# Kernel optimization log

Hardware: AMD Instinct MI355X
Metric: run time of the kernel (lower is better)

The kernel has to match this reference:

```python
import jax, jax.numpy as jnp
import numpy as np

WINDOW_SIZE = 11
SIGMA = 1.5
C1 = 0.01 ** 2
C2 = 0.03 ** 2


def _gaussian_window(window_size, sigma, channel, dtype):
    x = np.arange(window_size)
    g = np.exp(-((x - window_size // 2) ** 2) / (2.0 * sigma ** 2))
    g = g / g.sum()
    w2d = np.outer(g, g).astype(np.float32)  # [K,K]
    # depthwise kernel: [C, 1, K, K] (OIHW with feature_group_count=C)
    w = np.broadcast_to(w2d, (channel, 1, window_size, window_size))
    return jnp.asarray(w, dtype=dtype)


def _blur(x, window, channel):
    pad = WINDOW_SIZE // 2
    return jax.lax.conv_general_dilated(
        x, window,
        window_strides=(1, 1),
        padding=[(pad, pad), (pad, pad)],
        dimension_numbers=('NCHW', 'OIHW', 'NCHW'),
        feature_group_count=channel,
    )


def setup_inputs() -> dict:
    key = jax.random.key(0)
    k1, k2 = jax.random.split(key)
    shape = (16, 3, 512, 512)
    img1 = jax.random.uniform(k1, shape, dtype=jnp.float32)
    img2 = jax.random.uniform(k2, shape, dtype=jnp.float32)
    return {"img1": img1, "img2": img2}


def reference(img1, img2):
    channel = img1.shape[1]
    window = _gaussian_window(WINDOW_SIZE, SIGMA, channel, img1.dtype)

    mu1 = _blur(img1, window, channel)
    mu2 = _blur(img2, window, channel)
    mu1_sq = mu1 * mu1
    mu2_sq = mu2 * mu2
    mu1_mu2 = mu1 * mu2

    sigma1_sq = _blur(img1 * img1, window, channel) - mu1_sq
    sigma2_sq = _blur(img2 * img2, window, channel) - mu2_sq
    sigma12 = _blur(img1 * img2, window, channel) - mu1_mu2

    ssim_map = ((2.0 * mu1_mu2 + C1) * (2.0 * sigma12 + C2)) / (
        (mu1_sq + mu2_sq + C1) * (sigma1_sq + sigma2_sq + C2))
    return jnp.mean(ssim_map)  # size_average=True
```

## Files before the change

kernel.cpp:

```cpp
#include <hip/hip_runtime.h>
#include <math.h>

typedef float v2 __attribute__((ext_vector_type(2)));

#define SCALE 1073741824.0
#define NPIX 12582912.0
#define C1f 1e-4f
#define C2f 9e-4f

struct Wts {
    float w[11];
    v2 hp[12];
};

__device__ __forceinline__ v2 sp(float x) { v2 r; r.x = x; r.y = x; return r; }
__device__ __forceinline__ v2 f2(v2 a, v2 b, v2 c) {
    return __builtin_elementwise_fma(a, b, c);
}

#define LOADP(Abuf, Bbuf, grow) do {                                        \
    int rc_ = (grow); rc_ = rc_ < 0 ? 0 : (rc_ > 511 ? 511 : rc_);          \
    const float* ra_ = baseA + rc_ * 512;                                   \
    const float* rb_ = baseB + rc_ * 512;                                   \
    _Pragma("unroll") for (int k_ = 0; k_ < 7; ++k_) {                      \
        Abuf[k_] = *(const v2*)(ra_ + off[k_]);                             \
        Bbuf[k_] = *(const v2*)(rb_ + off[k_]);                             \
    } } while (0)

#define HPM(Abuf, Bbuf, PH, mval) do {                                      \
    v2 hS_ = sp(0.f), hD_ = sp(0.f), hP_ = sp(0.f), hM_ = sp(0.f);          \
    _Pragma("unroll") for (int j_ = 0; j_ < 12; ++j_) {                     \
        const int e_ = j_ + 1;                                              \
        const float xa_ = (e_ & 1) ? Abuf[e_ >> 1].y : Abuf[e_ >> 1].x;     \
        const float xb_ = (e_ & 1) ? Bbuf[e_ >> 1].y : Bbuf[e_ >> 1].x;     \
        const float u_ = xa_ + xb_, v_ = xa_ - xb_;                         \
        hS_ = f2(hpl[j_], sp(u_), hS_);                                     \
        hD_ = f2(hpl[j_], sp(v_), hD_);                                     \
        hP_ = f2(hpl[j_], sp(u_ * u_), hP_);                                \
        hM_ = f2(hpl[j_], sp(v_ * v_), hM_);                                \
    }                                                                       \
    const v2 mm_ = sp(mval);                                                \
    rS[PH] = hS_ * mm_; rD[PH] = hD_ * mm_;                                 \
    rP[PH] = hP_ * mm_; rM[PH] = hM_ * mm_; } while (0)

#define VOUTM(PH, vmval) do {                                               \
    v2 S_ = sp(0.f), D_ = sp(0.f), P_ = sp(0.f), M_ = sp(0.f);              \
    _Pragma("unroll") for (int k_ = 0; k_ < 11; ++k_) {                     \
        const int q_ = ((PH) + 1 + k_) % 12;                                \
        const v2 wk_ = sp(W.w[k_]);                                         \
        S_ = f2(wk_, rS[q_], S_); D_ = f2(wk_, rD[q_], D_);                 \
        P_ = f2(wk_, rP[q_], P_); M_ = f2(wk_, rM[q_], M_);                 \
    }                                                                       \
    const v2 ss_ = S_ * S_, dd_ = D_ * D_;                                  \
    const v2 mu12_  = (ss_ - dd_) * sp(0.25f);                              \
    const v2 musq_  = (ss_ + dd_) * sp(0.5f);                               \
    const v2 sig12_ = (P_ - M_) * sp(0.25f) - mu12_;                        \
    const v2 sigsm_ = (P_ + M_) * sp(0.5f) - musq_;                         \
    const v2 num_ = (sp(2.f) * mu12_ + sp(C1f)) * (sp(2.f) * sig12_ + sp(C2f)); \
    const v2 den_ = (musq_ + sp(C1f)) * (sigsm_ + sp(C2f));                 \
    v2 r_;                                                                  \
    r_.x = __builtin_amdgcn_rcpf(den_.x);                                   \
    r_.y = __builtin_amdgcn_rcpf(den_.y);                                   \
    r_ = r_ * (sp(2.f) - den_ * r_);                                        \
    loc = f2(num_ * sp(vmval), r_, loc); } while (0)

#define PSTEP(PH, PAR) do {                                                 \
    const float m_ = (X >= 0 && X < 512) ? 1.f : 0.f;                       \
    if (PAR) { HPM(A1, B1, PH, m_); LOADP(A1, B1, X + 2); }                 \
    else     { HPM(A0, B0, PH, m_); LOADP(A0, B0, X + 2); }                 \
    ++X;                                                                    \
    __builtin_amdgcn_sched_barrier(0); } while (0)

#define MSTEP(PH, PAR) do {                                                 \
    const float vm_ = (X - 6 < 512) ? 1.f : 0.f;                            \
    VOUTM(PH, vm_);                                                         \
    const float m_ = (X < 512) ? 1.f : 0.f;                                 \
    if (PAR) { HPM(A1, B1, PH, m_); LOADP(A1, B1, X + 2); }                 \
    else     { HPM(A0, B0, PH, m_); LOADP(A0, B0, X + 2); }                 \
    ++X;                                                                    \
    __builtin_amdgcn_sched_barrier(0); } while (0)

__global__ __launch_bounds__(256, 2) void ssim_main(
    const float* __restrict__ img1, const float* __restrict__ img2,
    unsigned long long* __restrict__ acc, Wts W)
{
    __shared__ float red[4];
    const int tid = threadIdx.x;
    const int lane = tid & 63;
    const int wv = tid >> 6;
    const int r0 = blockIdx.x * 48;
    const int plane = blockIdx.y;
    const int c = wv * 128 + 2 * lane;

    const float* baseA = img1 + (size_t)plane * 262144;
    const float* baseB = img2 + (size_t)plane * 262144;

    int off[7];
#pragma unroll
    for (int k = 0; k < 7; ++k) {
        int o = c - 6 + 2 * k;
        off[k] = o < 0 ? 0 : (o > 510 ? 510 : o);
    }
    v2 hpl[12];
#pragma unroll
    for (int j = 0; j < 12; ++j) {
        const int col = c - 5 + j;
        hpl[j] = (col >= 0 && col < 512) ? W.hp[j] : sp(0.f);
    }

    v2 rS[12], rD[12], rP[12], rM[12];
    v2 A0[7], B0[7], A1[7], B1[7];
    v2 loc = sp(0.f);

    int X = r0 - 5;
    LOADP(A0, B0, r0 - 5);
    LOADP(A1, B1, r0 - 4);
    __builtin_amdgcn_sched_barrier(0);

    PSTEP(0, 0);  PSTEP(1, 1);  PSTEP(2, 0);  PSTEP(3, 1);
    PSTEP(4, 0);  PSTEP(5, 1);  PSTEP(6, 0);  PSTEP(7, 1);
    PSTEP(8, 0);  PSTEP(9, 1);  PSTEP(10, 0);

    for (int b = 0; b < 4; ++b) {
        MSTEP(11, 1); MSTEP(0, 0);  MSTEP(1, 1);  MSTEP(2, 0);
        MSTEP(3, 1);  MSTEP(4, 0);  MSTEP(5, 1);  MSTEP(6, 0);
        MSTEP(7, 1);  MSTEP(8, 0);  MSTEP(9, 1);  MSTEP(10, 0);
    }

    float l = loc.x + loc.y;
#pragma unroll
    for (int o2 = 32; o2; o2 >>= 1)
        l += __shfl_down(l, o2, 64);
    if (lane == 0) red[wv] = l;
    __syncthreads();
    if (tid == 0) {
        const float bs = red[0] + red[1] + red[2] + red[3];
        const unsigned long long q =
            (unsigned long long)__double2ll_rn((double)bs * SCALE);
        atomicAdd(acc, q);
    }
}

__global__ void ssim_final(const unsigned long long* __restrict__ acc,
                           float* __restrict__ out)
{
    if (threadIdx.x == 0)
        out[0] = (float)((double)(*acc) * (1.0 / SCALE) / NPIX);
}

extern "C" void kernel_launch(void* const* d_in, const int* in_sizes, int n_in,
                              void* d_out, int out_size, void* d_ws, size_t ws_size,
                              hipStream_t stream) {
    const float* img1 = (const float*)d_in[0];
    const float* img2 = (const float*)d_in[1];
    float* out = (float*)d_out;
    unsigned long long* acc = (unsigned long long*)d_ws;

    double g[11], ssum = 0.0;
    for (int i = 0; i < 11; ++i) {
        const double d = (double)(i - 5);
        g[i] = exp(-(d * d) / 4.5);
        ssum += g[i];
    }
    Wts W;
    for (int i = 0; i < 11; ++i) W.w[i] = (float)(g[i] / ssum);
    for (int j = 0; j < 12; ++j) {
        v2 p;
        p.x = (j <= 10) ? W.w[j] : 0.f;
        p.y = (j >= 1) ? W.w[j - 1] : 0.f;
        W.hp[j] = p;
    }

    hipMemsetAsync(d_ws, 0, sizeof(unsigned long long), stream);
    ssim_main<<<dim3(11, 48), 256, 0, stream>>>(img1, img2, acc, W);
    ssim_final<<<1, 64, 0, stream>>>(acc, out);
}
```

Measured before the change: 84.36 us.

## Stage image rows through double-buffered LDS and shrink row tiles

Each block now loads one row of both images per step with coalesced float4 global loads into a double-buffered LDS slot that carries zero-padded halos. Each thread then reads its 14-column window from LDS instead of issuing overlapping, clamped global loads, and the squared sum/difference terms are computed once per loaded element. Row tiles shrink from 48 to 36, which gives more blocks (15x48), and the launch bound rises to 3 blocks per CU. In exchange there is a __syncthreads every row step and more vertical halo recomputation per tile.

```diff
diff --git a/kernel.cpp b/kernel.cpp
--- a/kernel.cpp
+++ b/kernel.cpp
@@ -8,6 +8,9 @@
 #define C1f 1e-4f
 #define C2f 9e-4f
 
+#define IMG_STR  528
+#define SLOT_STR 1056
+
 struct Wts {
     float w[11];
     v2 hp[12];
@@ -18,30 +21,32 @@
     return __builtin_elementwise_fma(a, b, c);
 }
 
-#define LOADP(Abuf, Bbuf, grow) do {                                        \
-    int rc_ = (grow); rc_ = rc_ < 0 ? 0 : (rc_ > 511 ? 511 : rc_);          \
-    const float* ra_ = baseA + rc_ * 512;                                   \
-    const float* rb_ = baseB + rc_ * 512;                                   \
+#define HPM(PH, SLR) do {                                                   \
+    const float* rp_ = &rowbuf[(SLR) * SLOT_STR] + lds_rd;                  \
+    v2 ca_[7], cb_[7];                                                      \
     _Pragma("unroll") for (int k_ = 0; k_ < 7; ++k_) {                      \
-        Abuf[k_] = *(const v2*)(ra_ + off[k_]);                             \
-        Bbuf[k_] = *(const v2*)(rb_ + off[k_]);                             \
-    } } while (0)
-
-#define HPM(Abuf, Bbuf, PH, mval) do {                                      \
+        ca_[k_] = *(const v2*)(rp_ + 2 * k_);                               \
+        cb_[k_] = *(const v2*)(rp_ + IMG_STR + 2 * k_);                     \
+    }                                                                       \
+    v2 uS_[7], uD_[7], uP_[7], uM_[7];                                      \
+    _Pragma("unroll") for (int k_ = 0; k_ < 7; ++k_) {                      \
+        uS_[k_] = ca_[k_] + cb_[k_];                                        \
+        uD_[k_] = ca_[k_] - cb_[k_];                                        \
+        uP_[k_] = uS_[k_] * uS_[k_];                                        \
+        uM_[k_] = uD_[k_] * uD_[k_];                                        \
+    }                                                                       \
     v2 hS_ = sp(0.f), hD_ = sp(0.f), hP_ = sp(0.f), hM_ = sp(0.f);          \
     _Pragma("unroll") for (int j_ = 0; j_ < 12; ++j_) {                     \
-        const int e_ = j_ + 1;                                              \
-        const float xa_ = (e_ & 1) ? Abuf[e_ >> 1].y : Abuf[e_ >> 1].x;     \
-        const float xb_ = (e_ & 1) ? Bbuf[e_ >> 1].y : Bbuf[e_ >> 1].x;     \
-        const float u_ = xa_ + xb_, v_ = xa_ - xb_;                         \
-        hS_ = f2(hpl[j_], sp(u_), hS_);                                     \
-        hD_ = f2(hpl[j_], sp(v_), hD_);                                     \
-        hP_ = f2(hpl[j_], sp(u_ * u_), hP_);                                \
-        hM_ = f2(hpl[j_], sp(v_ * v_), hM_);                                \
-    }                                                                       \
-    const v2 mm_ = sp(mval);                                                \
-    rS[PH] = hS_ * mm_; rD[PH] = hD_ * mm_;                                 \
-    rP[PH] = hP_ * mm_; rM[PH] = hM_ * mm_; } while (0)
+        const int e_ = j_ + 1, ch_ = e_ >> 1;                               \
+        v2 bS_, bD_, bP_, bM_;                                              \
+        if (e_ & 1) { bS_ = sp(uS_[ch_].y); bD_ = sp(uD_[ch_].y);           \
+                      bP_ = sp(uP_[ch_].y); bM_ = sp(uM_[ch_].y); }         \
+        else        { bS_ = sp(uS_[ch_].x); bD_ = sp(uD_[ch_].x);           \
+                      bP_ = sp(uP_[ch_].x); bM_ = sp(uM_[ch_].x); }         \
+        hS_ = f2(W.hp[j_], bS_, hS_); hD_ = f2(W.hp[j_], bD_, hD_);         \
+        hP_ = f2(W.hp[j_], bP_, hP_); hM_ = f2(W.hp[j_], bM_, hM_);         \
+    }                                                                       \
+    rS[PH] = hS_; rD[PH] = hD_; rP[PH] = hP_; rM[PH] = hM_; } while (0)
 
 #define VOUTM(PH, vmval) do {                                               \
     v2 S_ = sp(0.f), D_ = sp(0.f), P_ = sp(0.f), M_ = sp(0.f);              \
@@ -64,67 +69,88 @@
     r_ = r_ * (sp(2.f) - den_ * r_);                                        \
     loc = f2(num_ * sp(vmval), r_, loc); } while (0)
 
-#define PSTEP(PH, PAR) do {                                                 \
-    const float m_ = (X >= 0 && X < 512) ? 1.f : 0.f;                       \
-    if (PAR) { HPM(A1, B1, PH, m_); LOADP(A1, B1, X + 2); }                 \
-    else     { HPM(A0, B0, PH, m_); LOADP(A0, B0, X + 2); }                 \
-    ++X;                                                                    \
-    __builtin_amdgcn_sched_barrier(0); } while (0)
-
-#define MSTEP(PH, PAR) do {                                                 \
-    const float vm_ = (X - 6 < 512) ? 1.f : 0.f;                            \
-    VOUTM(PH, vm_);                                                         \
-    const float m_ = (X < 512) ? 1.f : 0.f;                                 \
-    if (PAR) { HPM(A1, B1, PH, m_); LOADP(A1, B1, X + 2); }                 \
-    else     { HPM(A0, B0, PH, m_); LOADP(A0, B0, X + 2); }                 \
-    ++X;                                                                    \
-    __builtin_amdgcn_sched_barrier(0); } while (0)
-
-__global__ __launch_bounds__(256, 2) void ssim_main(
+#define STEP(PH, SLR, SLW, scur, DOV) do {                                  \
+    const int grw_ = r0 - 4 + (scur);                                       \
+    const float mw_ = ((unsigned)grw_ < 512u) ? 1.f : 0.f;                  \
+    float4 w4_;                                                             \
+    w4_.x = sreg.x * mw_; w4_.y = sreg.y * mw_;                             \
+    w4_.z = sreg.z * mw_; w4_.w = sreg.w * mw_;                             \
+    *(float4*)(&rowbuf[(SLW) * SLOT_STR] + lds_wr) = w4_;                   \
+    {   const int grl_ = r0 - 3 + (scur);                                   \
+        const int rc_ = grl_ < 0 ? 0 : (grl_ > 511 ? 511 : grl_);           \
+        sreg = *(const float4*)(sbase + rc_ * 512 + scol);                  \
+    }                                                                       \
+    HPM(PH, SLR);                                                           \
+    if (DOV) {                                                              \
+        const float vm_ = (r0 + (scur) - 11 < 512) ? 1.f : 0.f;             \
+        VOUTM(PH, vm_);                                                     \
+    }                                                                       \
+    __builtin_amdgcn_sched_barrier(0);                                      \
+    __syncthreads();                                                        \
+} while (0)
+
+__global__ __launch_bounds__(256, 3) void ssim_main(
     const float* __restrict__ img1, const float* __restrict__ img2,
     unsigned long long* __restrict__ acc, Wts W)
 {
+    __shared__ float rowbuf[2 * SLOT_STR];
     __shared__ float red[4];
+
     const int tid = threadIdx.x;
     const int lane = tid & 63;
     const int wv = tid >> 6;
-    const int r0 = blockIdx.x * 48;
+    const int r0 = blockIdx.x * 36;
     const int plane = blockIdx.y;
-    const int c = wv * 128 + 2 * lane;
 
     const float* baseA = img1 + (size_t)plane * 262144;
     const float* baseB = img2 + (size_t)plane * 262144;
 
-    int off[7];
-#pragma unroll
-    for (int k = 0; k < 7; ++k) {
-        int o = c - 6 + 2 * k;
-        off[k] = o < 0 ? 0 : (o > 510 ? 510 : o);
-    }
-    v2 hpl[12];
-#pragma unroll
-    for (int j = 0; j < 12; ++j) {
-        const int col = c - 5 + j;
-        hpl[j] = (col >= 0 && col < 512) ? W.hp[j] : sp(0.f);
+    const int simg = tid >> 7;
+    const int scol = 4 * (tid & 127);
+    const float* sbase = simg ? baseB : baseA;
+    const int lds_wr = simg * IMG_STR + 8 + scol;
+    const int lds_rd = 2 + 2 * tid;
+
+    if (tid < 32) {
+        const int s_ = tid >> 4, rest = tid & 15;
+        const int i_ = rest >> 3, p_ = rest & 7;
+        rowbuf[s_ * SLOT_STR + i_ * IMG_STR + p_] = 0.f;
+        rowbuf[s_ * SLOT_STR + i_ * IMG_STR + 520 + p_] = 0.f;
     }
 
     v2 rS[12], rD[12], rP[12], rM[12];
-    v2 A0[7], B0[7], A1[7], B1[7];
     v2 loc = sp(0.f);
-
-    int X = r0 - 5;
-    LOADP(A0, B0, r0 - 5);
-    LOADP(A1, B1, r0 - 4);
-    __builtin_amdgcn_sched_barrier(0);
-
-    PSTEP(0, 0);  PSTEP(1, 1);  PSTEP(2, 0);  PSTEP(3, 1);
-    PSTEP(4, 0);  PSTEP(5, 1);  PSTEP(6, 0);  PSTEP(7, 1);
-    PSTEP(8, 0);  PSTEP(9, 1);  PSTEP(10, 0);
-
-    for (int b = 0; b < 4; ++b) {
-        MSTEP(11, 1); MSTEP(0, 0);  MSTEP(1, 1);  MSTEP(2, 0);
-        MSTEP(3, 1);  MSTEP(4, 0);  MSTEP(5, 1);  MSTEP(6, 0);
-        MSTEP(7, 1);  MSTEP(8, 0);  MSTEP(9, 1);  MSTEP(10, 0);
+    float4 sreg;
+
+    {
+        const int gr_ = r0 - 5;
+        const float m_ = ((unsigned)gr_ < 512u) ? 1.f : 0.f;
+        const int rc_ = gr_ < 0 ? 0 : gr_;
+        const float4 t_ = *(const float4*)(sbase + rc_ * 512 + scol);
+        float4 w_;
+        w_.x = t_.x * m_; w_.y = t_.y * m_; w_.z = t_.z * m_; w_.w = t_.w * m_;
+        *(float4*)(&rowbuf[1 * SLOT_STR] + lds_wr) = w_;
+    }
+    {
+        const int gr_ = r0 - 4;
+        const int rc_ = gr_ < 0 ? 0 : gr_;
+        sreg = *(const float4*)(sbase + rc_ * 512 + scol);
+    }
+    __syncthreads();
+
+    STEP(0, 1, 0, 0, 0);  STEP(1, 0, 1, 1, 0);  STEP(2, 1, 0, 2, 0);
+    STEP(3, 0, 1, 3, 0);  STEP(4, 1, 0, 4, 0);  STEP(5, 0, 1, 5, 0);
+    STEP(6, 1, 0, 6, 0);  STEP(7, 0, 1, 7, 0);  STEP(8, 1, 0, 8, 0);
+    STEP(9, 0, 1, 9, 0);  STEP(10, 1, 0, 10, 0);
+
+    for (int b_ = 0; b_ < 3; ++b_) {
+        const int sb = 11 + 12 * b_;
+        STEP(11, 0, 1, sb + 0, 1);  STEP(0, 1, 0, sb + 1, 1);
+        STEP(1, 0, 1, sb + 2, 1);   STEP(2, 1, 0, sb + 3, 1);
+        STEP(3, 0, 1, sb + 4, 1);   STEP(4, 1, 0, sb + 5, 1);
+        STEP(5, 0, 1, sb + 6, 1);   STEP(6, 1, 0, sb + 7, 1);
+        STEP(7, 0, 1, sb + 8, 1);   STEP(8, 1, 0, sb + 9, 1);
+        STEP(9, 0, 1, sb + 10, 1);  STEP(10, 1, 0, sb + 11, 1);
     }
 
     float l = loc.x + loc.y;
@@ -172,6 +198,6 @@
     }
 
     hipMemsetAsync(d_ws, 0, sizeof(unsigned long long), stream);
-    ssim_main<<<dim3(11, 48), 256, 0, stream>>>(img1, img2, acc, W);
+    ssim_main<<<dim3(15, 48), 256, 0, stream>>>(img1, img2, acc, W);
     ssim_final<<<1, 64, 0, stream>>>(acc, out);
 }
```

After: 89.97 us. 6.7% more time.

## Stage rows through per-wave LDS ring with coalesced float4 loads

Applied to the files above, without the earlier changes.

Each wave now loads its row strip (both images, with a halo) as coalesced float4 global loads, stores it into a 4-slot per-wave LDS ring, and reads its 7-pair window from LDS. Boundary masking moves into the LDS store, so per-lane column weights and row masks disappear from the math path. Rows per block drop from 48 to 32, giving a 16x48 grid for better CU coverage. Per-wave atomics replace the block-level shared reduction. This adds LDS traffic and relies on wave-synchronous LDS ordering with no barrier between write and read.

```diff
diff --git a/kernel.cpp b/kernel.cpp
--- a/kernel.cpp
+++ b/kernel.cpp
@@ -8,6 +8,10 @@
 #define C1f 1e-4f
 #define C2f 9e-4f
 
+#define IMG_OFF 144
+#define SLOT_STR 288
+#define WAVE_STR 1152
+
 struct Wts {
     float w[11];
     v2 hp[12];
@@ -18,32 +22,50 @@
     return __builtin_elementwise_fma(a, b, c);
 }
 
-#define LOADP(Abuf, Bbuf, grow) do {                                        \
+#define GLD(RP, RS, grow) do {                                              \
     int rc_ = (grow); rc_ = rc_ < 0 ? 0 : (rc_ > 511 ? 511 : rc_);          \
-    const float* ra_ = baseA + rc_ * 512;                                   \
-    const float* rb_ = baseB + rc_ * 512;                                   \
+    RP = *(const float4*)(pgl + (size_t)rc_ * 512);                         \
+    if (sec) RS = *(const float4*)(sgl + (size_t)rc_ * 512);                \
+} while (0)
+
+#define SWRITE(SLW, RP, RS, grw) do {                                       \
+    const float rm_ = ((unsigned)(grw) < 512u) ? 1.f : 0.f;                 \
+    float4 o_;                                                              \
+    o_.x = RP.x * (pm.x * rm_); o_.y = RP.y * (pm.y * rm_);                 \
+    o_.z = RP.z * (pm.z * rm_); o_.w = RP.w * (pm.w * rm_);                 \
+    *(float4*)(pwr + (SLW) * SLOT_STR) = o_;                                \
+    if (sec) {                                                              \
+        float4 s_;                                                          \
+        s_.x = RS.x * (sm.x * rm_); s_.y = RS.y * (sm.y * rm_);             \
+        s_.z = RS.z * (sm.z * rm_); s_.w = RS.w * (sm.w * rm_);             \
+        *(float4*)(swr + (SLW) * SLOT_STR) = s_;                            \
+    }                                                                       \
+} while (0)
+
+#define HPLOAD(SLR) do {                                                    \
+    const float* rp_ = rdp + (SLR) * SLOT_STR;                              \
     _Pragma("unroll") for (int k_ = 0; k_ < 7; ++k_) {                      \
-        Abuf[k_] = *(const v2*)(ra_ + off[k_]);                             \
-        Bbuf[k_] = *(const v2*)(rb_ + off[k_]);                             \
-    } } while (0)
-
-#define HPM(Abuf, Bbuf, PH, mval) do {                                      \
+        ca[k_] = *(const v2*)(rp_ + 2 * k_);                                \
+        cb[k_] = *(const v2*)(rp_ + IMG_OFF + 2 * k_);                      \
+    }                                                                       \
+} while (0)
+
+#define HPMATH(PH) do {                                                     \
     v2 hS_ = sp(0.f), hD_ = sp(0.f), hP_ = sp(0.f), hM_ = sp(0.f);          \
     _Pragma("unroll") for (int j_ = 0; j_ < 12; ++j_) {                     \
-        const int e_ = j_ + 1;                                              \
-        const float xa_ = (e_ & 1) ? Abuf[e_ >> 1].y : Abuf[e_ >> 1].x;     \
-        const float xb_ = (e_ & 1) ? Bbuf[e_ >> 1].y : Bbuf[e_ >> 1].x;     \
+        const int e_ = j_ + 1, ch_ = e_ >> 1;                               \
+        const float xa_ = (e_ & 1) ? ca[ch_].y : ca[ch_].x;                 \
+        const float xb_ = (e_ & 1) ? cb[ch_].y : cb[ch_].x;                 \
         const float u_ = xa_ + xb_, v_ = xa_ - xb_;                         \
-        hS_ = f2(hpl[j_], sp(u_), hS_);                                     \
-        hD_ = f2(hpl[j_], sp(v_), hD_);                                     \
-        hP_ = f2(hpl[j_], sp(u_ * u_), hP_);                                \
-        hM_ = f2(hpl[j_], sp(v_ * v_), hM_);                                \
-    }                                                                       \
-    const v2 mm_ = sp(mval);                                                \
-    rS[PH] = hS_ * mm_; rD[PH] = hD_ * mm_;                                 \
-    rP[PH] = hP_ * mm_; rM[PH] = hM_ * mm_; } while (0)
-
-#define VOUTM(PH, vmval) do {                                               \
+        hS_ = f2(W.hp[j_], sp(u_), hS_);                                    \
+        hD_ = f2(W.hp[j_], sp(v_), hD_);                                    \
+        hP_ = f2(W.hp[j_], sp(u_ * u_), hP_);                               \
+        hM_ = f2(W.hp[j_], sp(v_ * v_), hM_);                               \
+    }                                                                       \
+    rS[PH] = hS_; rD[PH] = hD_; rP[PH] = hP_; rM[PH] = hM_;                 \
+} while (0)
+
+#define VOUTM(PH) do {                                                      \
     v2 S_ = sp(0.f), D_ = sp(0.f), P_ = sp(0.f), M_ = sp(0.f);              \
     _Pragma("unroll") for (int k_ = 0; k_ < 11; ++k_) {                     \
         const int q_ = ((PH) + 1 + k_) % 12;                                \
@@ -62,81 +84,100 @@
     r_.x = __builtin_amdgcn_rcpf(den_.x);                                   \
     r_.y = __builtin_amdgcn_rcpf(den_.y);                                   \
     r_ = r_ * (sp(2.f) - den_ * r_);                                        \
-    loc = f2(num_ * sp(vmval), r_, loc); } while (0)
-
-#define PSTEP(PH, PAR) do {                                                 \
-    const float m_ = (X >= 0 && X < 512) ? 1.f : 0.f;                       \
-    if (PAR) { HPM(A1, B1, PH, m_); LOADP(A1, B1, X + 2); }                 \
-    else     { HPM(A0, B0, PH, m_); LOADP(A0, B0, X + 2); }                 \
-    ++X;                                                                    \
-    __builtin_amdgcn_sched_barrier(0); } while (0)
-
-#define MSTEP(PH, PAR) do {                                                 \
-    const float vm_ = (X - 6 < 512) ? 1.f : 0.f;                            \
-    VOUTM(PH, vm_);                                                         \
-    const float m_ = (X < 512) ? 1.f : 0.f;                                 \
-    if (PAR) { HPM(A1, B1, PH, m_); LOADP(A1, B1, X + 2); }                 \
-    else     { HPM(A0, B0, PH, m_); LOADP(A0, B0, X + 2); }                 \
-    ++X;                                                                    \
-    __builtin_amdgcn_sched_barrier(0); } while (0)
+    loc = f2(num_, r_, loc);                                                \
+} while (0)
+
+#define STEP(PH, SLR, SLW, PAR, scur, DOV) do {                             \
+    HPLOAD(SLR);                                                            \
+    if (PAR) { SWRITE(SLW, w1p, w1s, r0 - 3 + (scur)); }                    \
+    else     { SWRITE(SLW, w0p, w0s, r0 - 3 + (scur)); }                    \
+    if (DOV) VOUTM(PH);                                                     \
+    HPMATH(PH);                                                             \
+    if (PAR) { GLD(w1p, w1s, r0 - 1 + (scur)); }                            \
+    else     { GLD(w0p, w0s, r0 - 1 + (scur)); }                            \
+    __builtin_amdgcn_sched_barrier(0);                                      \
+} while (0)
 
 __global__ __launch_bounds__(256, 2) void ssim_main(
     const float* __restrict__ img1, const float* __restrict__ img2,
     unsigned long long* __restrict__ acc, Wts W)
 {
-    __shared__ float red[4];
+    __shared__ float rowbuf[4 * WAVE_STR];
+
     const int tid = threadIdx.x;
     const int lane = tid & 63;
     const int wv = tid >> 6;
-    const int r0 = blockIdx.x * 48;
+    const int r0 = blockIdx.x * 32;
     const int plane = blockIdx.y;
-    const int c = wv * 128 + 2 * lane;
+    const int c0w = wv * 128;
 
     const float* baseA = img1 + (size_t)plane * 262144;
     const float* baseB = img2 + (size_t)plane * 262144;
 
-    int off[7];
-#pragma unroll
-    for (int k = 0; k < 7; ++k) {
-        int o = c - 6 + 2 * k;
-        off[k] = o < 0 ? 0 : (o > 510 ? 510 : o);
-    }
-    v2 hpl[12];
-#pragma unroll
-    for (int j = 0; j < 12; ++j) {
-        const int col = c - 5 + j;
-        hpl[j] = (col >= 0 && col < 512) ? W.hp[j] : sp(0.f);
-    }
+    float* wbase = rowbuf + wv * WAVE_STR;
+    const float* rdp = wbase + 2 * lane + 2;
+
+    const int pimg = (lane < 36) ? 0 : 1;
+    const int pch  = (lane < 36) ? lane : lane - 36;
+    const int pg0  = c0w - 8 + 4 * pch;
+    const int pgc  = pg0 < 0 ? 0 : (pg0 > 508 ? 508 : pg0);
+    const float* pgl = (pimg ? baseB : baseA) + pgc;
+    float* pwr = wbase + pimg * IMG_OFF + 4 * pch;
+    float4 pm;
+    pm.x = (pg0 + 0 >= 0 && pg0 + 0 < 512) ? 1.f : 0.f;
+    pm.y = (pg0 + 1 >= 0 && pg0 + 1 < 512) ? 1.f : 0.f;
+    pm.z = (pg0 + 2 >= 0 && pg0 + 2 < 512) ? 1.f : 0.f;
+    pm.w = (pg0 + 3 >= 0 && pg0 + 3 < 512) ? 1.f : 0.f;
+
+    const bool sec = (lane < 8);
+    const int sch = 28 + lane;
+    const int sg0 = c0w - 8 + 4 * sch;
+    const int sgc = sg0 < 0 ? 0 : (sg0 > 508 ? 508 : sg0);
+    const float* sgl = baseB + sgc;
+    float* swr = wbase + IMG_OFF + 4 * sch;
+    float4 sm;
+    sm.x = (sg0 + 0 >= 0 && sg0 + 0 < 512) ? 1.f : 0.f;
+    sm.y = (sg0 + 1 >= 0 && sg0 + 1 < 512) ? 1.f : 0.f;
+    sm.z = (sg0 + 2 >= 0 && sg0 + 2 < 512) ? 1.f : 0.f;
+    sm.w = (sg0 + 3 >= 0 && sg0 + 3 < 512) ? 1.f : 0.f;
 
     v2 rS[12], rD[12], rP[12], rM[12];
-    v2 A0[7], B0[7], A1[7], B1[7];
+    v2 ca[7], cb[7];
     v2 loc = sp(0.f);
-
-    int X = r0 - 5;
-    LOADP(A0, B0, r0 - 5);
-    LOADP(A1, B1, r0 - 4);
+    float4 w0p, w0s, w1p, w1s;
+
+    GLD(w0p, w0s, r0 - 5);  SWRITE(0, w0p, w0s, r0 - 5);
+    GLD(w1p, w1s, r0 - 4);  SWRITE(1, w1p, w1s, r0 - 4);
+    GLD(w0p, w0s, r0 - 3);
+    GLD(w1p, w1s, r0 - 2);
     __builtin_amdgcn_sched_barrier(0);
 
-    PSTEP(0, 0);  PSTEP(1, 1);  PSTEP(2, 0);  PSTEP(3, 1);
-    PSTEP(4, 0);  PSTEP(5, 1);  PSTEP(6, 0);  PSTEP(7, 1);
-    PSTEP(8, 0);  PSTEP(9, 1);  PSTEP(10, 0);
-
-    for (int b = 0; b < 4; ++b) {
-        MSTEP(11, 1); MSTEP(0, 0);  MSTEP(1, 1);  MSTEP(2, 0);
-        MSTEP(3, 1);  MSTEP(4, 0);  MSTEP(5, 1);  MSTEP(6, 0);
-        MSTEP(7, 1);  MSTEP(8, 0);  MSTEP(9, 1);  MSTEP(10, 0);
-    }
+    STEP(0, 0, 2, 0, 0, 0);  STEP(1, 1, 3, 1, 1, 0);  STEP(2, 2, 0, 0, 2, 0);
+    STEP(3, 3, 1, 1, 3, 0);  STEP(4, 0, 2, 0, 4, 0);  STEP(5, 1, 3, 1, 5, 0);
+    STEP(6, 2, 0, 0, 6, 0);  STEP(7, 3, 1, 1, 7, 0);  STEP(8, 0, 2, 0, 8, 0);
+    STEP(9, 1, 3, 1, 9, 0);  STEP(10, 2, 0, 0, 10, 0);
+
+    for (int b = 0; b < 2; ++b) {
+        const int sb = 11 + 12 * b;
+        STEP(11, 3, 1, 1, sb + 0, 1);  STEP(0, 0, 2, 0, sb + 1, 1);
+        STEP(1, 1, 3, 1, sb + 2, 1);   STEP(2, 2, 0, 0, sb + 3, 1);
+        STEP(3, 3, 1, 1, sb + 4, 1);   STEP(4, 0, 2, 0, sb + 5, 1);
+        STEP(5, 1, 3, 1, sb + 6, 1);   STEP(6, 2, 0, 0, sb + 7, 1);
+        STEP(7, 3, 1, 1, sb + 8, 1);   STEP(8, 0, 2, 0, sb + 9, 1);
+        STEP(9, 1, 3, 1, sb + 10, 1);  STEP(10, 2, 0, 0, sb + 11, 1);
+    }
+    STEP(11, 3, 1, 1, 35, 1);  STEP(0, 0, 2, 0, 36, 1);
+    STEP(1, 1, 3, 1, 37, 1);   STEP(2, 2, 0, 0, 38, 1);
+    STEP(3, 3, 1, 1, 39, 1);   STEP(4, 0, 2, 0, 40, 1);
+    STEP(5, 1, 3, 1, 41, 1);   STEP(6, 2, 0, 0, 42, 1);
 
     float l = loc.x + loc.y;
 #pragma unroll
     for (int o2 = 32; o2; o2 >>= 1)
         l += __shfl_down(l, o2, 64);
-    if (lane == 0) red[wv] = l;
-    __syncthreads();
-    if (tid == 0) {
-        const float bs = red[0] + red[1] + red[2] + red[3];
+    if (lane == 0) {
         const unsigned long long q =
-            (unsigned long long)__double2ll_rn((double)bs * SCALE);
+            (unsigned long long)__double2ll_rn((double)l * SCALE);
         atomicAdd(acc, q);
     }
 }
@@ -172,6 +213,6 @@
     }
 
     hipMemsetAsync(d_ws, 0, sizeof(unsigned long long), stream);
-    ssim_main<<<dim3(11, 48), 256, 0, stream>>>(img1, img2, acc, W);
+    ssim_main<<<dim3(16, 48), 256, 0, stream>>>(img1, img2, acc, W);
     ssim_final<<<1, 64, 0, stream>>>(acc, out);
 }
```

Result: slower. 319.7 us (+279.0%).

## Process rows in pairs with split vertical sums and retile to 37-row strips

Applied to the files above, without the earlier changes.

The row loop is restructured so each step loads two input rows at once. It computes one full vertical output, then a partial vertical sum for the next output that is finished after the new horizontal row is pushed. Rows per block drop from 48 to 37 and the grid grows from 11 to 14 row blocks, so there are more blocks and less over-computation past the image edge. The prologue-free loop starts with zeroed ring registers and masks outputs by time index. The cost is more outstanding load registers per step and extra warm-up rows per block.

```diff
diff --git a/kernel.cpp b/kernel.cpp
--- a/kernel.cpp
+++ b/kernel.cpp
@@ -18,67 +18,87 @@
     return __builtin_elementwise_fma(a, b, c);
 }
 
-#define LOADP(Abuf, Bbuf, grow) do {                                        \
-    int rc_ = (grow); rc_ = rc_ < 0 ? 0 : (rc_ > 511 ? 511 : rc_);          \
-    const float* ra_ = baseA + rc_ * 512;                                   \
-    const float* rb_ = baseB + rc_ * 512;                                   \
-    _Pragma("unroll") for (int k_ = 0; k_ < 7; ++k_) {                      \
-        Abuf[k_] = *(const v2*)(ra_ + off[k_]);                             \
-        Bbuf[k_] = *(const v2*)(rb_ + off[k_]);                             \
-    } } while (0)
-
-#define HPM(Abuf, Bbuf, PH, mval) do {                                      \
-    v2 hS_ = sp(0.f), hD_ = sp(0.f), hP_ = sp(0.f), hM_ = sp(0.f);          \
-    _Pragma("unroll") for (int j_ = 0; j_ < 12; ++j_) {                     \
-        const int e_ = j_ + 1;                                              \
-        const float xa_ = (e_ & 1) ? Abuf[e_ >> 1].y : Abuf[e_ >> 1].x;     \
-        const float xb_ = (e_ & 1) ? Bbuf[e_ >> 1].y : Bbuf[e_ >> 1].x;     \
-        const float u_ = xa_ + xb_, v_ = xa_ - xb_;                         \
-        hS_ = f2(hpl[j_], sp(u_), hS_);                                     \
-        hD_ = f2(hpl[j_], sp(v_), hD_);                                     \
-        hP_ = f2(hpl[j_], sp(u_ * u_), hP_);                                \
-        hM_ = f2(hpl[j_], sp(v_ * v_), hM_);                                \
-    }                                                                       \
-    const v2 mm_ = sp(mval);                                                \
-    rS[PH] = hS_ * mm_; rD[PH] = hD_ * mm_;                                 \
-    rP[PH] = hP_ * mm_; rM[PH] = hM_ * mm_; } while (0)
-
-#define VOUTM(PH, vmval) do {                                               \
-    v2 S_ = sp(0.f), D_ = sp(0.f), P_ = sp(0.f), M_ = sp(0.f);              \
-    _Pragma("unroll") for (int k_ = 0; k_ < 11; ++k_) {                     \
-        const int q_ = ((PH) + 1 + k_) % 12;                                \
-        const v2 wk_ = sp(W.w[k_]);                                         \
-        S_ = f2(wk_, rS[q_], S_); D_ = f2(wk_, rD[q_], D_);                 \
-        P_ = f2(wk_, rP[q_], P_); M_ = f2(wk_, rM[q_], M_);                 \
-    }                                                                       \
-    const v2 ss_ = S_ * S_, dd_ = D_ * D_;                                  \
+#define SSIMTAIL(S_, D_, P_, M_, tt) do {                                   \
+    const v2 ss_ = (S_) * (S_), dd_ = (D_) * (D_);                          \
     const v2 mu12_  = (ss_ - dd_) * sp(0.25f);                              \
     const v2 musq_  = (ss_ + dd_) * sp(0.5f);                               \
-    const v2 sig12_ = (P_ - M_) * sp(0.25f) - mu12_;                        \
-    const v2 sigsm_ = (P_ + M_) * sp(0.5f) - musq_;                         \
-    const v2 num_ = (sp(2.f) * mu12_ + sp(C1f)) * (sp(2.f) * sig12_ + sp(C2f)); \
+    const v2 sig12_ = ((P_) - (M_)) * sp(0.25f) - mu12_;                    \
+    const v2 sigsm_ = ((P_) + (M_)) * sp(0.5f) - musq_;                     \
+    const v2 num_ = (sp(2.f)*mu12_ + sp(C1f)) * (sp(2.f)*sig12_ + sp(C2f)); \
     const v2 den_ = (musq_ + sp(C1f)) * (sigsm_ + sp(C2f));                 \
     v2 r_;                                                                  \
     r_.x = __builtin_amdgcn_rcpf(den_.x);                                   \
     r_.y = __builtin_amdgcn_rcpf(den_.y);                                   \
     r_ = r_ * (sp(2.f) - den_ * r_);                                        \
-    loc = f2(num_ * sp(vmval), r_, loc); } while (0)
+    const float vm_ = ((tt) >= 11 && (r0 + (tt) - 11) < 512) ? 1.f : 0.f;   \
+    loc = f2(num_ * sp(vm_), r_, loc);                                      \
+} while (0)
 
-#define PSTEP(PH, PAR) do {                                                 \
-    const float m_ = (X >= 0 && X < 512) ? 1.f : 0.f;                       \
-    if (PAR) { HPM(A1, B1, PH, m_); LOADP(A1, B1, X + 2); }                 \
-    else     { HPM(A0, B0, PH, m_); LOADP(A0, B0, X + 2); }                 \
-    ++X;                                                                    \
-    __builtin_amdgcn_sched_barrier(0); } while (0)
+#define VOUTFULL(PH, tt) do {                                               \
+    v2 S0 = sp(0.f), D0 = sp(0.f), P0 = sp(0.f), M0 = sp(0.f);              \
+    _Pragma("unroll") for (int k = 0; k < 11; ++k) {                        \
+        const int q = ((PH) + 1 + k) % 12;                                  \
+        const v2 wk = sp(W.w[k]);                                           \
+        S0 = f2(wk, rS[q], S0); D0 = f2(wk, rD[q], D0);                     \
+        P0 = f2(wk, rP[q], P0); M0 = f2(wk, rM[q], M0);                     \
+    }                                                                       \
+    SSIMTAIL(S0, D0, P0, M0, tt);                                           \
+} while (0)
 
-#define MSTEP(PH, PAR) do {                                                 \
-    const float vm_ = (X - 6 < 512) ? 1.f : 0.f;                            \
-    VOUTM(PH, vm_);                                                         \
-    const float m_ = (X < 512) ? 1.f : 0.f;                                 \
-    if (PAR) { HPM(A1, B1, PH, m_); LOADP(A1, B1, X + 2); }                 \
-    else     { HPM(A0, B0, PH, m_); LOADP(A0, B0, X + 2); }                 \
-    ++X;                                                                    \
-    __builtin_amdgcn_sched_barrier(0); } while (0)
+#define HPUSH(PH, A, B, grow) do {                                          \
+    v2 hS = sp(0.f), hD = sp(0.f), hP = sp(0.f), hM = sp(0.f);              \
+    _Pragma("unroll") for (int j = 0; j < 12; ++j) {                        \
+        const int e = j + 1;                   \
+        const float xa = (e & 1) ? A[e >> 1].y : A[e >> 1].x;               \
+        const float xb = (e & 1) ? B[e >> 1].y : B[e >> 1].x;               \
+        const float u = xa + xb, v = xa - xb;                               \
+        hS = f2(hpl[j], sp(u), hS);                                         \
+        hD = f2(hpl[j], sp(v), hD);                                         \
+        hP = f2(hpl[j], sp(u * u), hP);                                     \
+        hM = f2(hpl[j], sp(v * v), hM);                                     \
+    }                                                                       \
+    const float m = ((unsigned)(grow) < 512u) ? 1.f : 0.f;                  \
+    const v2 mm = sp(m);                                                    \
+    rS[PH] = hS * mm; rD[PH] = hD * mm;                                     \
+    rP[PH] = hP * mm; rM[PH] = hM * mm;                                     \
+} while (0)
+
+#define PAIR(J, PA, PB) do {                                                \
+    const int ta = 12 * it + 2 * (J);                                       \
+    const int ga = r0 - 5 + ta;                                             \
+    const int gb = ga + 1;                                                  \
+    const int rca = ga < 0 ? 0 : (ga > 511 ? 511 : ga);                     \
+    const int rcb = gb < 0 ? 0 : (gb > 511 ? 511 : gb);                     \
+    const float* raa = baseA + rca * 512;                                   \
+    const float* rba = baseB + rca * 512;                                   \
+    const float* rab = baseA + rcb * 512;                                   \
+    const float* rbb = baseB + rcb * 512;                                   \
+    _Pragma("unroll") for (int k = 0; k < 7; ++k) {                         \
+        a0[k] = *(const v2*)(raa + off[k]);                                 \
+        b0[k] = *(const v2*)(rba + off[k]);                                 \
+    }                                                                       \
+    _Pragma("unroll") for (int k = 0; k < 7; ++k) {                         \
+        a1[k] = *(const v2*)(rab + off[k]);                                 \
+        b1[k] = *(const v2*)(rbb + off[k]);                                 \
+    }                                                                       \
+    VOUTFULL(PA, ta);                                                       \
+    v2 S1 = sp(0.f), D1 = sp(0.f), P1 = sp(0.f), M1 = sp(0.f);              \
+    _Pragma("unroll") for (int k = 0; k < 10; ++k) {                        \
+        const int q = ((PB) + 1 + k) % 12;              \
+        const v2 wk = sp(W.w[k]);                                           \
+        S1 = f2(wk, rS[q], S1); D1 = f2(wk, rD[q], D1);                     \
+        P1 = f2(wk, rP[q], P1); M1 = f2(wk, rM[q], M1);                     \
+    }                                                                       \
+    HPUSH(PA, a0, b0, ga);                                                  \
+    {                                                                       \
+        const v2 w10 = sp(W.w[10]);          \
+        S1 = f2(w10, rS[PA], S1); D1 = f2(w10, rD[PA], D1);                 \
+        P1 = f2(w10, rP[PA], P1); M1 = f2(w10, rM[PA], M1);                 \
+        SSIMTAIL(S1, D1, P1, M1, ta + 1);                                   \
+    }                                                                       \
+    HPUSH(PB, a1, b1, gb);                                                  \
+    __builtin_amdgcn_sched_barrier(0);       \
+} while (0)
 
 __global__ __launch_bounds__(256, 2) void ssim_main(
     const float* __restrict__ img1, const float* __restrict__ img2,
@@ -88,7 +108,7 @@
     const int tid = threadIdx.x;
     const int lane = tid & 63;
     const int wv = tid >> 6;
-    const int r0 = blockIdx.x * 48;
+    const int r0 = blockIdx.x * 37;
     const int plane = blockIdx.y;
     const int c = wv * 128 + 2 * lane;
 
@@ -109,22 +129,17 @@
     }
 
     v2 rS[12], rD[12], rP[12], rM[12];
-    v2 A0[7], B0[7], A1[7], B1[7];
+#pragma unroll
+    for (int q = 0; q < 12; ++q) {
+        rS[q] = sp(0.f); rD[q] = sp(0.f);
+        rP[q] = sp(0.f); rM[q] = sp(0.f);
+    }
+    v2 a0[7], b0[7], a1[7], b1[7];
     v2 loc = sp(0.f);
 
-    int X = r0 - 5;
-    LOADP(A0, B0, r0 - 5);
-    LOADP(A1, B1, r0 - 4);
-    __builtin_amdgcn_sched_barrier(0);
-
-    PSTEP(0, 0);  PSTEP(1, 1);  PSTEP(2, 0);  PSTEP(3, 1);
-    PSTEP(4, 0);  PSTEP(5, 1);  PSTEP(6, 0);  PSTEP(7, 1);
-    PSTEP(8, 0);  PSTEP(9, 1);  PSTEP(10, 0);
-
-    for (int b = 0; b < 4; ++b) {
-        MSTEP(11, 1); MSTEP(0, 0);  MSTEP(1, 1);  MSTEP(2, 0);
-        MSTEP(3, 1);  MSTEP(4, 0);  MSTEP(5, 1);  MSTEP(6, 0);
-        MSTEP(7, 1);  MSTEP(8, 0);  MSTEP(9, 1);  MSTEP(10, 0);
+    for (int it = 0; it < 4; ++it) {
+        PAIR(0, 0, 1);  PAIR(1, 2, 3);  PAIR(2, 4, 5);
+        PAIR(3, 6, 7);  PAIR(4, 8, 9);  PAIR(5, 10, 11);
     }
 
     float l = loc.x + loc.y;
@@ -172,6 +187,6 @@
     }
 
     hipMemsetAsync(d_ws, 0, sizeof(unsigned long long), stream);
-    ssim_main<<<dim3(11, 48), 256, 0, stream>>>(img1, img2, acc, W);
+    ssim_main<<<dim3(14, 48), 256, 0, stream>>>(img1, img2, acc, W);
     ssim_final<<<1, 64, 0, stream>>>(acc, out);
 }
```

After: 74.48 us. 1.13x faster.
